# Optimization experiments

Measured on AMD Instinct MI355X. Metric: run time of the kernel, lower is better.

Reference implementation:

```python
import jax, jax.numpy as jnp
import numpy as np
import math

LMAX = 8  # even real SH up to degree 8 -> K = 45 basis functions
BVALS = np.array([1.0, 2.0, 3.0], dtype=np.float32)


def _assoc_legendre(x, lmax):
    # associated Legendre P_l^m(x) for 0<=m<=l<=lmax via standard recurrences
    P = {(0, 0): jnp.ones_like(x)}
    s = jnp.sqrt(jnp.clip(1.0 - x * x, 0.0, 1.0))
    for m in range(1, lmax + 1):
        P[(m, m)] = -(2 * m - 1) * s * P[(m - 1, m - 1)]
    for m in range(0, lmax):
        P[(m + 1, m)] = (2 * m + 1) * x * P[(m, m)]
    for m in range(0, lmax + 1):
        for l in range(m + 2, lmax + 1):
            P[(l, m)] = ((2 * l - 1) * x * P[(l - 1, m)] - (l + m - 1) * P[(l - 2, m)]) / (l - m)
    return P


def _sh_degrees(lmax):
    # FuncSpace.n : degree l of each basis function (even degrees only)
    return np.array([l for l in range(0, lmax + 1, 2) for m in range(-l, l + 1)])


def real_sh_basis(dirs):
    # FuncSpace.harmonic_expansion: (..., 3) directions -> (..., K) real symmetric SH
    d = dirs / jnp.linalg.norm(dirs, axis=-1, keepdims=True)
    x, y, z = d[..., 0], d[..., 1], d[..., 2]
    phi = jnp.arctan2(y, x)
    P = _assoc_legendre(z, LMAX)  # cos(theta) = z
    cols = []
    for l in range(0, LMAX + 1, 2):
        for m in range(-l, l + 1):
            ma = abs(m)
            nrm = math.sqrt((2 * l + 1) / (4 * math.pi) * math.factorial(l - ma) / math.factorial(l + ma))
            if m < 0:
                cols.append(math.sqrt(2.0) * nrm * jnp.sin(ma * phi) * P[(l, ma)])
            elif m == 0:
                cols.append(nrm * P[(l, 0)])
            else:
                cols.append(math.sqrt(2.0) * nrm * jnp.cos(m * phi) * P[(l, m)])
    return jnp.stack(cols, axis=-1)


def _legendre_poly(t, lmax):
    # Legendre polynomials P_l(t), l = 0..lmax, shape (lmax+1, T)
    Ps = [jnp.ones_like(t), t]
    for n in range(1, lmax):
        Ps.append(((2 * n + 1) * t * Ps[n] - n * Ps[n - 1]) / (n + 1))
    return jnp.stack(Ps[: lmax + 1], axis=0)


def setup_inputs() -> dict:
    key = jax.random.key(0)
    k1, k2, k3 = jax.random.split(key, 3)
    N, F = 8192, 3
    return {
        "directs": jax.random.normal(k1, (N, F, 3), dtype=jnp.float32),
        "weights": jax.random.uniform(k2, (N, F), dtype=jnp.float32),
        "shapes": jax.random.uniform(k3, (N, F, 4), dtype=jnp.float32),
        "num_t": 1000,
    }


def reference(directs, weights, shapes, num_t):
    degrees = _sh_degrees(LMAX)                                  # (K,)
    l_ks, l_k_idx = np.unique(degrees, return_inverse=True)      # unique even degrees + map to K
    b = jnp.asarray(BVALS)                                       # (B,)
    t = jnp.linspace(0.0, 1.0, num_t)                            # (T,)
    t2 = t * t
    D_a, D_epar, D_eperp, z = (shapes[..., i] for i in range(4))  # each (N, F)
    bD = b[None, None, :, None]                                  # (1,1,B,1)
    # StandardModel kernel evaluations, batched over samples/fibers/bvals: (N,F,B,T)
    kern = (z[..., None, None] * jnp.exp(-bD * D_a[..., None, None] * t2)
            + (1.0 - z[..., None, None]) * jnp.exp(-bD * D_eperp[..., None, None]
                                                   - bD * (D_epar - D_eperp)[..., None, None] * t2))
    # trapezoid weights matching torch.trapz(y, dx=1/num_t) exactly
    w = jnp.full((num_t,), 1.0 / num_t).at[0].set(0.5 / num_t).at[-1].set(0.5 / num_t)
    P = _legendre_poly(t, int(l_ks.max()))[np.asarray(l_ks)]     # (L,T) at unique degrees
    rho = jnp.einsum('nfbt,lt->nbfl', kern * w, P)               # (N,B,F,L) rho_k integrals
    eigen_values = rho[..., np.asarray(l_k_idx)]                 # (N,B,F,K) broadcast to basis fns
    ODFtensor = real_sh_basis(directs)                           # (N,F,K)
    Stensor = jnp.einsum('nf,nbfk,nfk->nbk', weights, eigen_values, ODFtensor)  # sum over fibers
    return Stensor, ODFtensor, eigen_values
```

## Files before the change

kernel.cpp:

```cpp
#include <hip/hip_runtime.h>
#include <math.h>

#define FF 3
#define BB 3
#define KK 45
#define VOX 8
#define TPB 256
#define NT 18
#define NFIB (VOX*FF)
#define NRHO (VOX*FF*BB)

constexpr double csqrt(double x) {
    double g = x > 1.0 ? x : 1.0;
    for (int i = 0; i < 64; ++i) g = 0.5 * (g + x / g);
    return g;
}

struct Tab { float d[5][NT]; };
constexpr Tab make_tab() {
    Tab t{};
    for (int li = 0; li < 5; ++li) {
        const int l = 2 * li;
        double kfact = 1.0;
        for (int k = 0; k < NT; ++k) {
            if (k > 0) kfact *= (double)k;
            double c = 0.0;
            if (2 * k >= l) {
                double num = 1.0, den = 1.0;
                for (int j = 0; j < l / 2; ++j)  num *= (double)(2 * k - 2 * j);
                for (int j = 0; j <= l / 2; ++j) den *= (double)(2 * k + 1 + 2 * j);
                c = num / den;
            }
            t.d[li][k] = (float)(((k & 1) ? -1.0 : 1.0) * c / kfact);
        }
    }
    return t;
}
static constexpr Tab HOST_TAB = make_tab();
__constant__ Tab TAB = HOST_TAB;

struct KTab {
    float nrm[KK];
    unsigned char lidx[KK];
    unsigned char ma[KK];
    unsigned char neg[KK];
};
constexpr KTab make_ktab() {
    KTab t{};
    int k = 0;
    for (int l = 0; l <= 8; l += 2) {
        for (int m = -l; m <= l; ++m, ++k) {
            const int ma = m < 0 ? -m : m;
            double prod = 1.0;
            for (int i = l - ma + 1; i <= l + ma; ++i) prod *= (double)i;
            double nrm = csqrt((double)(2 * l + 1) * 0.07957747154594767 / prod);
            if (m != 0) nrm *= csqrt(2.0);
            t.nrm[k]  = (float)nrm;
            t.lidx[k] = (unsigned char)(l / 2);
            t.ma[k]   = (unsigned char)ma;
            t.neg[k]  = (unsigned char)(m < 0 ? 1 : 0);
        }
    }
    return t;
}
static constexpr KTab HOST_KT = make_ktab();
__constant__ KTab KT = HOST_KT;

__device__ __forceinline__ void eval_I(float a, float I[5]) {
    #pragma unroll
    for (int li = 0; li < 5; ++li) {
        float acc = TAB.d[li][NT - 1];
        #pragma unroll
        for (int k = NT - 2; k >= 0; --k)
            acc = fmaf(acc, a, TAB.d[li][k]);
        I[li] = acc;
    }
}

__global__ __launch_bounds__(TPB) void fused_sim_kernel(
    const float* __restrict__ directs,
    const float* __restrict__ weights,
    const float* __restrict__ shapes,
    const int*   __restrict__ num_t_p,
    float* __restrict__ outS,
    float* __restrict__ outODF,
    float* __restrict__ outEig,
    int N)
{
    const int n0  = blockIdx.x * VOX;
    const int tid = threadIdx.x;
    const bool full = (n0 + VOX <= N);

    __shared__ float P_s[NFIB][25];
    __shared__ float cm_s[NFIB][9];
    __shared__ float sm_s[NFIB][9];
    __shared__ float rho_s[NRHO][5];
    __shared__ float sh_s[VOX * FF * KK];
    __shared__ float w_s[NFIB];

    if (tid < NFIB) {
        const int v = tid / FF;
        const int f = tid % FF;
        const int n = n0 + v;
        if (n < N) {
            const float dx = directs[(n * FF + f) * 3 + 0];
            const float dy = directs[(n * FF + f) * 3 + 1];
            const float dz = directs[(n * FF + f) * 3 + 2];
            const float inv = 1.0f / sqrtf(dx * dx + dy * dy + dz * dz);
            const float x = dx * inv, y = dy * inv, z = dz * inv;
            float s2 = 1.0f - z * z;
            s2 = fminf(fmaxf(s2, 0.0f), 1.0f);
            const float s = sqrtf(s2);

            const float rxy2 = x * x + y * y;
            float cphi = 1.0f, sphi = 0.0f;
            if (rxy2 > 0.0f) {
                const float ir = 1.0f / sqrtf(rxy2);
                cphi = x * ir;
                sphi = y * ir;
            }

            float cm = 1.0f, sm = 0.0f;
            #pragma unroll
            for (int m = 0; m <= 8; ++m) {
                cm_s[tid][m] = cm;
                sm_s[tid][m] = sm;
                const float cn = cm * cphi - sm * sphi;
                const float sn = sm * cphi + cm * sphi;
                cm = cn; sm = sn;
            }

            float pmm = 1.0f;
            #pragma unroll
            for (int ma = 0; ma <= 8; ++ma) {
                if (ma > 0) pmm *= -(float)(2 * ma - 1) * s;
                if ((ma & 1) == 0)
                    P_s[tid][(ma / 2) * (ma / 2) + ma] = pmm;
                float pa = pmm;
                float pb = (float)(2 * ma + 1) * z * pa;
                if (ma + 1 <= 8 && ((ma + 1) & 1) == 0)
                    P_s[tid][((ma + 1) / 2) * ((ma + 1) / 2) + ma] = pb;
                #pragma unroll
                for (int ll = ma + 2; ll <= 8; ++ll) {
                    const float invd = 1.0f / (float)(ll - ma);
                    const float pn = ((float)(2 * ll - 1) * z * pb
                                      - (float)(ll + ma - 1) * pa) * invd;
                    pa = pb; pb = pn;
                    if ((ll & 1) == 0)
                        P_s[tid][(ll / 2) * (ll / 2) + ma] = pn;
                }
            }

            w_s[tid] = weights[n * FF + f];
        }
    }

    if (tid >= 64 && tid < 64 + NRHO) {
        const int w  = tid - 64;
        const int fi = w / BB;
        const int bi = w % BB;
        const int n  = n0 + fi / FF;
        const int f  = fi % FF;
        if (n < N) {
            const float bval = (float)(bi + 1);

            const float D_a     = shapes[(n * FF + f) * 4 + 0];
            const float D_epar  = shapes[(n * FF + f) * 4 + 1];
            const float D_eperp = shapes[(n * FF + f) * 4 + 2];
            const float zf      = shapes[(n * FF + f) * 4 + 3];

            const float bA = bval * D_a;
            const float bE = bval * (D_epar - D_eperp);
            const float zc = (1.0f - zf) * __expf(-bval * D_eperp);

            const float T     = (float)num_t_p[0];
            const float h     = 1.0f / (T - 1.0f);
            const float scale = (T - 1.0f) / T;
            const float h212  = h * h * (1.0f / 12.0f);

            float IA[5], IE[5];
            eval_I(bA, IA);
            eval_I(bE, IE);
            const float eA = __expf(-bA);
            const float eE = __expf(-bE);

            #pragma unroll
            for (int li = 0; li < 5; ++li) {
                const int   l   = 2 * li;
                const float pl1 = 0.5f * (float)(l * (l + 1));
                const float QA = IA[li] + h212 * eA * (pl1 - 2.0f * bA);
                const float QE = IE[li] + h212 * eE * (pl1 - 2.0f * bE);
                rho_s[w][li] = scale * (zf * QA + zc * QE);
            }
        }
    }

    __syncthreads();

    {
        float4* dst = (float4*)(outODF + (size_t)n0 * (FF * KK));
        for (int q = tid; q < VOX * FF * KK / 4; q += TPB) {
            float4 out;
            float* oc = &out.x;
            #pragma unroll
            for (int j = 0; j < 4; ++j) {
                const int e  = 4 * q + j;
                const int fi = e / KK;
                const int k  = e % KK;
                const int lidx = KT.lidx[k];
                const int ma   = KT.ma[k];
                const float tr = KT.neg[k] ? sm_s[fi][ma] : cm_s[fi][ma];
                const float val = KT.nrm[k] * tr * P_s[fi][lidx * lidx + ma];
                sh_s[e] = val;
                oc[j] = val;
            }
            if (full) {
                dst[q] = out;
            } else {
                #pragma unroll
                for (int j = 0; j < 4; ++j) {
                    const int e = 4 * q + j;
                    if (n0 + e / (FF * KK) < N)
                        outODF[(size_t)n0 * (FF * KK) + e] = oc[j];
                }
            }
        }
    }

    __syncthreads();

    {
        float4* dst = (float4*)(outEig + (size_t)n0 * (BB * FF * KK));
        for (int q = tid; q < VOX * BB * FF * KK / 4; q += TPB) {
            float4 out;
            float* oc = &out.x;
            #pragma unroll
            for (int j = 0; j < 4; ++j) {
                const int e  = 4 * q + j;
                const int v  = e / (BB * FF * KK);
                const int r  = e % (BB * FF * KK);
                const int bi = r / (FF * KK);
                const int f  = (r / KK) % FF;
                const int k  = r % KK;
                oc[j] = rho_s[(v * FF + f) * BB + bi][KT.lidx[k]];
            }
            if (full) {
                dst[q] = out;
            } else {
                #pragma unroll
                for (int j = 0; j < 4; ++j) {
                    const int e = 4 * q + j;
                    if (n0 + e / (BB * FF * KK) < N)
                        outEig[(size_t)n0 * (BB * FF * KK) + e] = oc[j];
                }
            }
        }
    }

    {
        float4* dst = (float4*)(outS + (size_t)n0 * (BB * KK));
        for (int q = tid; q < VOX * BB * KK / 4; q += TPB) {
            float4 out;
            float* oc = &out.x;
            #pragma unroll
            for (int j = 0; j < 4; ++j) {
                const int e  = 4 * q + j;
                const int v  = e / (BB * KK);
                const int r  = e % (BB * KK);
                const int bi = r / KK;
                const int k  = r % KK;
                const int lidx = KT.lidx[k];
                float ssum = 0.0f;
                #pragma unroll
                for (int f = 0; f < FF; ++f) {
                    const int fi = v * FF + f;
                    ssum = fmaf(w_s[fi] * rho_s[fi * BB + bi][lidx],
                                sh_s[fi * KK + k], ssum);
                }
                oc[j] = ssum;
            }
            if (full) {
                dst[q] = out;
            } else {
                #pragma unroll
                for (int j = 0; j < 4; ++j) {
                    const int e = 4 * q + j;
                    if (n0 + e / (BB * KK) < N)
                        outS[(size_t)n0 * (BB * KK) + e] = oc[j];
                }
            }
        }
    }
}

extern "C" void kernel_launch(void* const* d_in, const int* in_sizes, int n_in,
                              void* d_out, int out_size, void* d_ws, size_t ws_size,
                              hipStream_t stream) {
    const float* directs = (const float*)d_in[0];
    const float* weights = (const float*)d_in[1];
    const float* shapes  = (const float*)d_in[2];
    const int*   num_t   = (const int*)d_in[3];

    const int N = in_sizes[0] / (FF * 3);

    float* outS   = (float*)d_out;
    float* outODF = outS + (size_t)N * BB * KK;
    float* outEig = outODF + (size_t)N * FF * KK;

    const int blocks = (N + VOX - 1) / VOX;
    fused_sim_kernel<<<blocks, TPB, 0, stream>>>(directs, weights, shapes, num_t,
                                                 outS, outODF, outEig, N);
}
```

Measured before the change: 73.93 us.

## Compute SH rows and eigen tiles per-thread into shared, then bulk-copy outputs

The per-fiber threads now keep the Legendre and trig values in registers and write the full 45-entry SH row straight to shared memory. The rho threads likewise write the expanded eigenvalue tile and weight-premultiplied rho values to shared memory. Each output is then a plain float4 copy from shared memory, which removes one __syncthreads and the per-element div/mod index math. The S reduction uses a constant lookup table of packed offsets. The trade-off is more register pressure and serial work in the 24 and 72 producer threads, while the other threads sit idle during that phase.

```diff
diff --git a/kernel.cpp b/kernel.cpp
--- a/kernel.cpp
+++ b/kernel.cpp
@@ -63,8 +63,21 @@
     }
     return t;
 }
-static constexpr KTab HOST_KT = make_ktab();
-__constant__ KTab KT = HOST_KT;
+static constexpr KTab HKT = make_ktab();
+
+struct STab { unsigned short v[BB * KK]; };
+constexpr STab make_stab() {
+    STab t{};
+    KTab kt = make_ktab();
+    for (int r = 0; r < BB * KK; ++r) {
+        const int bi = r / KK;
+        const int k  = r % KK;
+        t.v[r] = (unsigned short)((unsigned)(bi * 5 + kt.lidx[k]) | ((unsigned)k << 8));
+    }
+    return t;
+}
+static constexpr STab HOST_STAB = make_stab();
+__constant__ STab TS = HOST_STAB;
 
 __device__ __forceinline__ void eval_I(float a, float I[5]) {
     #pragma unroll
@@ -91,17 +104,13 @@
     const int tid = threadIdx.x;
     const bool full = (n0 + VOX <= N);
 
-    __shared__ float P_s[NFIB][25];
-    __shared__ float cm_s[NFIB][9];
-    __shared__ float sm_s[NFIB][9];
-    __shared__ float rho_s[NRHO][5];
-    __shared__ float sh_s[VOX * FF * KK];
-    __shared__ float w_s[NFIB];
+    __shared__ __align__(16) float sh_s[NFIB * KK];
+    __shared__ __align__(16) float eig_s[VOX * BB * FF * KK];
+    __shared__ __align__(16) float wrho_s[NRHO * 5];
 
     if (tid < NFIB) {
-        const int v = tid / FF;
         const int f = tid % FF;
-        const int n = n0 + v;
+        const int n = n0 + tid / FF;
         if (n < N) {
             const float dx = directs[(n * FF + f) * 3 + 0];
             const float dy = directs[(n * FF + f) * 3 + 1];
@@ -120,26 +129,28 @@
                 sphi = y * ir;
             }
 
+            float cmv[9], smv[9];
             float cm = 1.0f, sm = 0.0f;
             #pragma unroll
             for (int m = 0; m <= 8; ++m) {
-                cm_s[tid][m] = cm;
-                sm_s[tid][m] = sm;
+                cmv[m] = cm;
+                smv[m] = sm;
                 const float cn = cm * cphi - sm * sphi;
                 const float sn = sm * cphi + cm * sphi;
                 cm = cn; sm = sn;
             }
 
+            float Preg[25];
             float pmm = 1.0f;
             #pragma unroll
             for (int ma = 0; ma <= 8; ++ma) {
                 if (ma > 0) pmm *= -(float)(2 * ma - 1) * s;
                 if ((ma & 1) == 0)
-                    P_s[tid][(ma / 2) * (ma / 2) + ma] = pmm;
+                    Preg[(ma / 2) * (ma / 2) + ma] = pmm;
                 float pa = pmm;
                 float pb = (float)(2 * ma + 1) * z * pa;
                 if (ma + 1 <= 8 && ((ma + 1) & 1) == 0)
-                    P_s[tid][((ma + 1) / 2) * ((ma + 1) / 2) + ma] = pb;
+                    Preg[((ma + 1) / 2) * ((ma + 1) / 2) + ma] = pb;
                 #pragma unroll
                 for (int ll = ma + 2; ll <= 8; ++ll) {
                     const float invd = 1.0f / (float)(ll - ma);
@@ -147,11 +158,18 @@
                                       - (float)(ll + ma - 1) * pa) * invd;
                     pa = pb; pb = pn;
                     if ((ll & 1) == 0)
-                        P_s[tid][(ll / 2) * (ll / 2) + ma] = pn;
+                        Preg[(ll / 2) * (ll / 2) + ma] = pn;
                 }
             }
 
-            w_s[tid] = weights[n * FF + f];
+            float* shrow = sh_s + tid * KK;
+            #pragma unroll
+            for (int k = 0; k < KK; ++k) {
+                const int   lidx = HKT.lidx[k];
+                const int   ma   = HKT.ma[k];
+                const float tr   = HKT.neg[k] ? smv[ma] : cmv[ma];
+                shrow[k] = HKT.nrm[k] * tr * Preg[lidx * lidx + ma];
+            }
         }
     }
 
@@ -159,15 +177,17 @@
         const int w  = tid - 64;
         const int fi = w / BB;
         const int bi = w % BB;
-        const int n  = n0 + fi / FF;
+        const int v  = fi / FF;
         const int f  = fi % FF;
+        const int n  = n0 + v;
         if (n < N) {
             const float bval = (float)(bi + 1);
 
-            const float D_a     = shapes[(n * FF + f) * 4 + 0];
-            const float D_epar  = shapes[(n * FF + f) * 4 + 1];
-            const float D_eperp = shapes[(n * FF + f) * 4 + 2];
-            const float zf      = shapes[(n * FF + f) * 4 + 3];
+            const float4 sp4 = *(const float4*)(shapes + (size_t)(n * FF + f) * 4);
+            const float D_a     = sp4.x;
+            const float D_epar  = sp4.y;
+            const float D_eperp = sp4.z;
+            const float zf      = sp4.w;
 
             const float bA = bval * D_a;
             const float bE = bval * (D_epar - D_eperp);
@@ -184,100 +204,78 @@
             const float eA = __expf(-bA);
             const float eE = __expf(-bE);
 
+            float rho[5];
             #pragma unroll
             for (int li = 0; li < 5; ++li) {
                 const int   l   = 2 * li;
                 const float pl1 = 0.5f * (float)(l * (l + 1));
                 const float QA = IA[li] + h212 * eA * (pl1 - 2.0f * bA);
                 const float QE = IE[li] + h212 * eE * (pl1 - 2.0f * bE);
-                rho_s[w][li] = scale * (zf * QA + zc * QE);
-            }
+                rho[li] = scale * (zf * QA + zc * QE);
+            }
+
+            const float wt = weights[n * FF + f];
+            #pragma unroll
+            for (int li = 0; li < 5; ++li)
+                wrho_s[w * 5 + li] = wt * rho[li];
+
+            float* er = eig_s + (v * (BB * FF) + bi * FF + f) * KK;
+            #pragma unroll
+            for (int k = 0; k < KK; ++k)
+                er[k] = rho[HKT.lidx[k]];
         }
     }
 
     __syncthreads();
+
+    {
+        float4* dst = (float4*)(outEig + (size_t)n0 * (BB * FF * KK));
+        const float4* src = (const float4*)eig_s;
+        if (full) {
+            for (int q = tid; q < VOX * BB * FF * KK / 4; q += TPB)
+                dst[q] = src[q];
+        } else {
+            for (int e = tid; e < VOX * BB * FF * KK; e += TPB)
+                if (n0 + e / (BB * FF * KK) < N)
+                    outEig[(size_t)n0 * (BB * FF * KK) + e] = eig_s[e];
+        }
+    }
 
     {
         float4* dst = (float4*)(outODF + (size_t)n0 * (FF * KK));
-        for (int q = tid; q < VOX * FF * KK / 4; q += TPB) {
-            float4 out;
-            float* oc = &out.x;
-            #pragma unroll
-            for (int j = 0; j < 4; ++j) {
-                const int e  = 4 * q + j;
-                const int fi = e / KK;
-                const int k  = e % KK;
-                const int lidx = KT.lidx[k];
-                const int ma   = KT.ma[k];
-                const float tr = KT.neg[k] ? sm_s[fi][ma] : cm_s[fi][ma];
-                const float val = KT.nrm[k] * tr * P_s[fi][lidx * lidx + ma];
-                sh_s[e] = val;
-                oc[j] = val;
-            }
-            if (full) {
-                dst[q] = out;
-            } else {
-                #pragma unroll
-                for (int j = 0; j < 4; ++j) {
-                    const int e = 4 * q + j;
-                    if (n0 + e / (FF * KK) < N)
-                        outODF[(size_t)n0 * (FF * KK) + e] = oc[j];
-                }
-            }
-        }
-    }
-
-    __syncthreads();
-
-    {
-        float4* dst = (float4*)(outEig + (size_t)n0 * (BB * FF * KK));
-        for (int q = tid; q < VOX * BB * FF * KK / 4; q += TPB) {
-            float4 out;
-            float* oc = &out.x;
-            #pragma unroll
-            for (int j = 0; j < 4; ++j) {
-                const int e  = 4 * q + j;
-                const int v  = e / (BB * FF * KK);
-                const int r  = e % (BB * FF * KK);
-                const int bi = r / (FF * KK);
-                const int f  = (r / KK) % FF;
-                const int k  = r % KK;
-                oc[j] = rho_s[(v * FF + f) * BB + bi][KT.lidx[k]];
-            }
-            if (full) {
-                dst[q] = out;
-            } else {
-                #pragma unroll
-                for (int j = 0; j < 4; ++j) {
-                    const int e = 4 * q + j;
-                    if (n0 + e / (BB * FF * KK) < N)
-                        outEig[(size_t)n0 * (BB * FF * KK) + e] = oc[j];
-                }
-            }
+        const float4* src = (const float4*)sh_s;
+        if (full) {
+            for (int q = tid; q < VOX * FF * KK / 4; q += TPB)
+                dst[q] = src[q];
+        } else {
+            for (int e = tid; e < VOX * FF * KK; e += TPB)
+                if (n0 + e / (FF * KK) < N)
+                    outODF[(size_t)n0 * (FF * KK) + e] = sh_s[e];
         }
     }
 
     {
         float4* dst = (float4*)(outS + (size_t)n0 * (BB * KK));
         for (int q = tid; q < VOX * BB * KK / 4; q += TPB) {
+            const int e0 = 4 * q;
+            int vv = (int)((unsigned)e0 / (unsigned)(BB * KK));
+            int r  = e0 - vv * (BB * KK);
+            const float* wrb = wrho_s + vv * (FF * BB * 5);
+            const float* shb = sh_s   + vv * (FF * KK);
             float4 out;
             float* oc = &out.x;
             #pragma unroll
             for (int j = 0; j < 4; ++j) {
-                const int e  = 4 * q + j;
-                const int v  = e / (BB * KK);
-                const int r  = e % (BB * KK);
-                const int bi = r / KK;
-                const int k  = r % KK;
-                const int lidx = KT.lidx[k];
+                if (r >= BB * KK) { r -= BB * KK; wrb += FF * BB * 5; shb += FF * KK; }
+                const unsigned ts = TS.v[r];
+                const float* wr = wrb + (ts & 0xffu);
+                const float* sp = shb + (ts >> 8);
                 float ssum = 0.0f;
-                #pragma unroll
-                for (int f = 0; f < FF; ++f) {
-                    const int fi = v * FF + f;
-                    ssum = fmaf(w_s[fi] * rho_s[fi * BB + bi][lidx],
-                                sh_s[fi * KK + k], ssum);
-                }
+                ssum = fmaf(wr[0],  sp[0],  ssum);
+                ssum = fmaf(wr[15], sp[45], ssum);
+                ssum = fmaf(wr[30], sp[90], ssum);
                 oc[j] = ssum;
+                ++r;
             }
             if (full) {
                 dst[q] = out;
```

After: 68.57 us. 7.2% less time.
